# Kernel tuning notes

Hardware: AMD Instinct MI355X
Metric: run time of the kernel (lower is better)

The kernel has to match this reference:

```python
import jax, jax.numpy as jnp
import numpy as np

HEADS = 8; DIM = 512; DHEAD = 64; INNER = HEADS * DHEAD
QB = 4; NTOK = 1024
GAMMA = 0.01; LAMBDA_REG = 0.001


def _ln(x, g, b, eps=1e-5):
    mu = x.mean(axis=-1, keepdims=True)
    var = x.var(axis=-1, keepdims=True)
    return (x - mu) / jnp.sqrt(var + eps) * g + b


def setup_inputs() -> dict:
    key = jax.random.key(0)
    ks = jax.random.split(key, 12)
    def w(k, shape, scale=0.02):
        return jax.random.normal(k, shape, dtype=jnp.float32) * scale
    return {
        'q': jax.random.normal(ks[0], (QB, NTOK, DIM), dtype=jnp.float32),
        'k': jax.random.normal(ks[1], (QB, NTOK, DIM), dtype=jnp.float32),
        'v': jax.random.normal(ks[2], (QB, NTOK, DIM), dtype=jnp.float32),
        'ln_in_g': jnp.ones((DIM,), jnp.float32),
        'ln_in_b': jnp.zeros((DIM,), jnp.float32),
        'W_in': w(ks[3], (DIM, INNER)),
        'wp_W1': w(ks[4], (2 * DHEAD, DHEAD)),
        'wp_b1': jnp.zeros((DHEAD,), jnp.float32),
        'wp_ln_g': jnp.ones((DHEAD,), jnp.float32),
        'wp_ln_b': jnp.zeros((DHEAD,), jnp.float32),
        'wp_W2': w(ks[5], (DHEAD, DHEAD // 2)),
        'wp_b2': jnp.zeros((DHEAD // 2,), jnp.float32),
        'wp_W3': w(ks[6], (DHEAD // 2, 3)),
        'wp_b3': jnp.zeros((3,), jnp.float32),
        'weight_temp': jnp.ones((1,), jnp.float32),
        'W_out': w(ks[7], (INNER, DIM)),
        'b_out': jnp.zeros((DIM,), jnp.float32),
    }


def _forward(q, k, v, ln_in_g, ln_in_b, W_in, wp_W1, wp_b1, wp_ln_g, wp_ln_b,
             wp_W2, wp_b2, wp_W3, wp_b3, weight_temp, W_out, b_out):
    def proj(t):  # [Q,N,DIM] -> [h,Q,N,d]
        y = _ln(t, ln_in_g, ln_in_b) @ W_in
        return y.reshape(t.shape[0], t.shape[1], HEADS, DHEAD).transpose(2, 0, 1, 3)
    f_q, f_k, f_v = proj(q), proj(k), proj(v)
    m = f_k.shape[2]
    sg = jax.lax.stop_gradient

    # --- cosine distance (clamped) ---
    dots = jnp.einsum('hqnd,hqmd->hqnm', f_q, f_k)
    n1 = jnp.linalg.norm(f_q, axis=-1, keepdims=True) + 1e-8   # [h,q,n,1]
    n2 = jnp.linalg.norm(f_k, axis=-1, keepdims=True) + 1e-8   # [h,q,m,1]
    cos = jnp.clip(dots / (n1 * jnp.swapaxes(n2, -1, -2)), -0.99, 0.99)

    # --- regularized covariance ---
    fkc = f_k - f_k.mean(axis=2, keepdims=True)
    fqc = f_q - f_q.mean(axis=-1, keepdims=True)
    cov = jnp.einsum('hqnd,hqmd->hqnm', fqc, fkc) / (DHEAD ** 0.5 + 1e-6)
    base_reg = LAMBDA_REG / max(m, 1)
    reg = jnp.where(jnp.std(cov, ddof=1) < 1e-6, base_reg * 10.0, base_reg)
    cov = jnp.clip(reg * cov, -50.0, 50.0)

    # --- margin-based variance (eval mode: adaptive_gamma = gamma) ---
    qn = f_q / jnp.maximum(jnp.linalg.norm(f_q, axis=-1, keepdims=True), 1e-6)
    kn = f_k / jnp.maximum(jnp.linalg.norm(f_k, axis=-1, keepdims=True), 1e-6)
    csim = jnp.clip(jnp.einsum('hqnd,hqmd->hqnm', qn, kn), -0.99, 0.99)
    margin = jnp.clip(GAMMA - csim, 0.0, 10.0)
    var_c = jnp.broadcast_to(margin.mean(axis=-1, keepdims=True), csim.shape)

    # --- dynamic per-head weight predictor (dropout off in eval) ---
    qg = f_q.mean(axis=(1, 2))          # [h,d]
    kg = f_k.mean(axis=(1, 2))
    feats = jnp.concatenate([qg, kg], axis=-1)          # [h,2d]
    h1 = jax.nn.relu(_ln(feats @ wp_W1 + wp_b1, wp_ln_g, wp_ln_b))
    h2 = jax.nn.relu(h1 @ wp_W2 + wp_b2)
    logits = jax.nn.softmax(h2 @ wp_W3 + wp_b3, axis=-1)  # Sequential ends with Softmax
    wt = jnp.clip(weight_temp, 0.1, 20.0)
    w = jax.nn.softmax(logits / wt, axis=-1)
    w = jnp.clip(w, 0.05, 0.8)
    w = w / w.sum(axis=-1, keepdims=True)                # [h,3]
    cw = w[:, 0].reshape(HEADS, 1, 1, 1)
    covw = w[:, 1].reshape(HEADS, 1, 1, 1)
    vw = w[:, 2].reshape(HEADS, 1, 1, 1)

    # --- normalize each component by its (detached) global std ---
    cn = sg(jnp.std(cos, ddof=1)) + 1e-6
    covn = sg(jnp.std(cov, ddof=1)) + 1e-6
    vn = sg(jnp.std(var_c, ddof=1)) + 1e-6
    cscale = jnp.where(cn < 1e-4, 0.1, 1.0)
    d2 = cw * (cos / cn * cscale) + covw * (cov / covn * 0.5) + vw * (var_c / vn * 0.5)
    dstd = jnp.std(d2, ddof=1)
    temp = jnp.where(dstd < 1e-6, 0.1, 0.3 + sg(dstd))
    d2 = d2 / jnp.clip(temp, 0.1, 5.0)

    attn = jax.nn.softmax(d2, axis=-1)
    out = jnp.einsum('hqnm,hqmd->hqnd', attn, f_v)
    out = out.transpose(1, 2, 0, 3).reshape(out.shape[1], out.shape[2], INNER)
    return out @ W_out + b_out


def reference(q, k, v, ln_in_g, ln_in_b, W_in, wp_W1, wp_b1, wp_ln_g, wp_ln_b,
              wp_W2, wp_b2, wp_W3, wp_b3, weight_temp, W_out, b_out):
    return _forward(q, k, v, ln_in_g, ln_in_b, W_in, wp_W1, wp_b1, wp_ln_g, wp_ln_b,
                    wp_W2, wp_b2, wp_W3, wp_b3, weight_temp, W_out, b_out)
```

## Files before the change

kernel.cpp:

```cpp
#include <hip/hip_runtime.h>
#include <math.h>

#define NH    8
#define NQB   4
#define NPAIR 32
#define NTOK  1024
#define DH    64
#define DIMX  512
#define NROWS (NPAIR*NTOK)

typedef __attribute__((ext_vector_type(8))) short short8;
typedef _Float16 half8 __attribute__((ext_vector_type(8)));
typedef __attribute__((ext_vector_type(4))) float f32x4;

__device__ __forceinline__ unsigned short f2bf(float x){
  unsigned u = __float_as_uint(x);
  u += 0x7fffu + ((u>>16)&1u);
  return (unsigned short)(u>>16);
}
__device__ __forceinline__ float bf2f(unsigned short h){
  return __uint_as_float(((unsigned)h)<<16);
}
__device__ __forceinline__ unsigned short f2h(float x){
  union{ _Float16 f; unsigned short u; } c; c.f = (_Float16)x; return c.u;
// ... 9 lines not shown
}
__device__ __forceinline__ void dma16(const void* g, void* l){
  __builtin_amdgcn_global_load_lds(
      (const __attribute__((address_space(1))) void*)g,
      (__attribute__((address_space(3))) void*)l, 16, 0, 0);
}

__device__ __forceinline__ size_t cidx(int r, int c){
  return ((((size_t)((r>>6)*8 + (c>>6)))*8 + ((c&63)>>3))*64 + (r&63))*8 + (c&7);
}
__device__ __forceinline__ size_t kidx(int p, int key, int dh){
  return ((((size_t)(p*16 + (key>>6)))*8 + (dh>>3))*64 + (key&63))*8 + (dh&7);
}


__global__ __launch_bounds__(256) void k_lnstats(const float* __restrict__ q,
    const float* __restrict__ k, const float* __restrict__ v,
    float* __restrict__ mu_rstd){
  int wid = threadIdx.x >> 6, lane = threadIdx.x & 63;
  int tok = blockIdx.x*4 + wid;
  const float* src = (tok < 4096) ? q : ((tok < 8192) ? k : v);
  int t = tok & 4095;
  const float4* p4 = (const float4*)(src + (size_t)t*DIMX) + lane*2;
  float4 a = p4[0], b = p4[1];
  float s  = a.x+a.y+a.z+a.w + b.x+b.y+b.z+b.w;
  float ss = a.x*a.x+a.y*a.y+a.z*a.z+a.w*a.w
           + b.x*b.x+b.y*b.y+b.z*b.z+b.w*b.w;
  #pragma unroll
  for (int off=32; off; off>>=1){ s += __shfl_down(s,off); ss += __shfl_down(ss,off); }
  if (lane==0){
    float mu = s*(1.0f/512.0f);
    float var = ss*(1.0f/512.0f) - mu*mu;
    mu_rstd[tok*2+0] = mu;
    mu_rstd[tok*2+1] = 1.0f/sqrtf(var + 1e-5f);
  }
}


__global__ __launch_bounds__(256) void k_splitW(const float* __restrict__ Wa,
    const float* __restrict__ Wb,
    unsigned short* __restrict__ Wth, unsigned short* __restrict__ Wtl,
    unsigned short* __restrict__ Woth, unsigned short* __restrict__ Wotl){
  __shared__ float tile[64][65];
  int z = blockIdx.z;
  const float* W = z ? Wb : Wa;
  unsigned short* oh_ = z ? Woth : Wth;
  unsigned short* ol_ = z ? Wotl : Wtl;
  int kb = blockIdx.x, nb = blockIdx.y, tid = threadIdx.x;
  #pragma unroll
  for (int it=0; it<4; ++it){
    int idx = tid + 256*it;
    int kr = idx>>4, c4 = idx&15;
    float4 vv = *(const float4*)(W + (size_t)(kb*64+kr)*DIMX + nb*64 + c4*4);
    tile[c4*4+0][kr]=vv.x; tile[c4*4+1][kr]=vv.y; tile[c4*4+2][kr]=vv.z; tile[c4*4+3][kr]=vv.w;
  }
  __syncthreads();
  #pragma unroll
  for (int it=0; it<4; ++it){
    int idx = tid + 256*it;
    int n = idx>>4, k4 = idx&15;
    size_t base = cidx(nb*64+n, kb*64+k4*4);
    ushort4 hv, lv;
    { float xx=tile[n][k4*4+0]; unsigned short hh=f2bf(xx); hv.x=hh; lv.x=f2bf(xx-bf2f(hh)); }
    { float xx=tile[n][k4*4+1]; unsigned short hh=f2bf(xx); hv.y=hh; lv.y=f2bf(xx-bf2f(hh)); }
    { float xx=tile[n][k4*4+2]; unsigned short hh=f2bf(xx); hv.z=hh; lv.z=f2bf(xx-bf2f(hh)); }
    { float xx=tile[n][k4*4+3]; unsigned short hh=f2bf(xx); hv.w=hh; lv.w=f2bf(xx-bf2f(hh)); }
    *(ushort4*)(oh_+base) = hv;
    *(ushort4*)(ol_+base) = lv;
  }
}


__global__ __launch_bounds__(256) void k_projmm(
    const float* __restrict__ q, const float* __restrict__ k, const float* __restrict__ v,
    const float* __restrict__ g, const float* __restrict__ bln,
    const unsigned short* __restrict__ Wth, const unsigned short* __restrict__ Wtl,
    const float* __restrict__ mu_rstd,
    unsigned short* __restrict__ fqh, unsigned short* __restrict__ fql,
    unsigned short* __restrict__ fkh, unsigned short* __restrict__ fkl,
    float* __restrict__ fv,
    double* __restrict__ qgs, double* __restrict__ nusum){
  __shared__ __align__(16) unsigned short Ahs[64*72];
  __shared__ __align__(16) unsigned short Als[64*72];
// ... 130 lines not shown
      for (int nt=0;nt<4;++nt){
        #pragma unroll
        for (int i=0;i<4;++i){
          int tglob = mb*64 + rbase + mt*16 + qd*4 + i;
          int qb = tglob>>10, n = tglob&1023;
          int p = head*4 + qb;
          int d = nt*16 + lm;
          fv[((size_t)(p*NTOK+n))*DH + d] = acc[mt][nt][i];
        }
      }
    }
  }
}


__global__ __launch_bounds__(256) void k_vT(const float* __restrict__ fv,
    unsigned short* __restrict__ fvTh, unsigned short* __restrict__ fvTl){
  __shared__ float tile[64][65];
  int mc = blockIdx.x, p = blockIdx.y, tid = threadIdx.x;
  #pragma unroll
  for (int it=0; it<4; ++it){
    int idx = tid + 256*it;
    int m = idx>>4, d4 = idx&15;
    float4 vv = *(const float4*)(fv + ((size_t)(p*NTOK + mc*64 + m)*DH + d4*4));
    tile[d4*4+0][m]=vv.x; tile[d4*4+1][m]=vv.y; tile[d4*4+2][m]=vv.z; tile[d4*4+3][m]=vv.w;
  }
  __syncthreads();
  #pragma unroll
  for (int it=0; it<2; ++it){
    int idx = tid + 256*it;
    int d = idx>>3, seg = idx&7;
    size_t base = ((((size_t)(p*16+mc))*8 + seg)*64 + d)*8;
    ushort4 h0,h1,l0,l1;
    { float xx=tile[d][seg*8+0]; unsigned short hh=f2h(xx); h0.x=hh; l0.x=f2h(xx-h2f(hh)); }
    { float xx=tile[d][seg*8+1]; unsigned short hh=f2h(xx); h0.y=hh; l0.y=f2h(xx-h2f(hh)); }
    { float xx=tile[d][seg*8+2]; unsigned short hh=f2h(xx); h0.z=hh; l0.z=f2h(xx-h2f(hh)); }
    { float xx=tile[d][seg*8+3]; unsigned short hh=f2h(xx); h0.w=hh; l0.w=f2h(xx-h2f(hh)); }
    { float xx=tile[d][seg*8+4]; unsigned short hh=f2h(xx); h1.x=hh; l1.x=f2h(xx-h2f(hh)); }
    { float xx=tile[d][seg*8+5]; unsigned short hh=f2h(xx); h1.y=hh; l1.y=f2h(xx-h2f(hh)); }
    { float xx=tile[d][seg*8+6]; unsigned short hh=f2h(xx); h1.z=hh; l1.z=f2h(xx-h2f(hh)); }
    { float xx=tile[d][seg*8+7]; unsigned short hh=f2h(xx); h1.w=hh; l1.w=f2h(xx-h2f(hh)); }
    *(ushort4*)(fvTh+base)   = h0;
    *(ushort4*)(fvTh+base+4) = h1;
    *(ushort4*)(fvTl+base)   = l0;
    *(ushort4*)(fvTl+base+4) = l1;
  }
}


__global__ __launch_bounds__(256) void k_rows(
    const unsigned short* __restrict__ fqh, const unsigned short* __restrict__ fql,
    const unsigned short* __restrict__ fkh, const unsigned short* __restrict__ fkl,
    const double* __restrict__ nusum,
    float* __restrict__ inv_na_q, float* __restrict__ muqA, float* __restrict__ tqA,
    float* __restrict__ inv_na_k, float* __restrict__ skA){
  int wid = threadIdx.x >> 6, lane = threadIdx.x & 63;
  int row = blockIdx.x*4 + wid;
  int p = row >> 10;
  int key = row & 1023;
  size_t ix = (size_t)row*DH + lane;
  float xq = bf2f(fqh[ix]) + bf2f(fql[ix]);
  float nv = (float)(nusum[(size_t)p*DH + lane] * (1.0/1024.0));
  float s = xq, ss = xq*xq, sd = xq*nv;
  #pragma unroll
  for (int off=32; off; off>>=1){
    s += __shfl_down(s,off); ss += __shfl_down(ss,off); sd += __shfl_down(sd,off);
  }
  if (lane==0){
    float nrm = sqrtf(ss);
    inv_na_q[row] = 1.0f/(nrm+1e-8f);
    muqA[row] = s*(1.0f/64.0f);
    tqA[row] = sd;
  }
  size_t ixk = kidx(p, key, lane);
  float xk = bf2f(fkh[ixk]) + bf2f(fkl[ixk]);
  float s2 = xk, ss2 = xk*xk;
  #pragma unroll
  for (int off=32; off; off>>=1){
    s2 += __shfl_down(s2,off); ss2 += __shfl_down(ss2,off);
  }
  if (lane==0){
    float nrm = sqrtf(ss2);
    inv_na_k[row] = 1.0f/(nrm+1e-8f);
    skA[row] = s2;
  }
}


__global__ __launch_bounds__(256) void k_wp(const double* __restrict__ qgs,
    const double* __restrict__ nusum,
    const float* __restrict__ W1, const float* __restrict__ b1,
    const float* __restrict__ lgv, const float* __restrict__ lbv,
    const float* __restrict__ W2, const float* __restrict__ b2,
    const float* __restrict__ W3, const float* __restrict__ b3,
    const float* __restrict__ wtemp, float* __restrict__ wp_out,
    float* __restrict__ Sarr){
  __shared__ float feats[8][128];
  __shared__ float h1[8][64];
  __shared__ float h2s[8][32];
  __shared__ float lgt[8][3];
  __shared__ float mv[8][2];
  int tid = threadIdx.x;
  for (int idx = tid; idx < 1024; idx += 256){
    int h = idx >> 7, i = idx & 127;
    double vv;
    if (i < 64){
      vv = qgs[h*64+i];
    } else {
      int d = i - 64;
      vv = nusum[(size_t)(h*4+0)*DH+d] + nusum[(size_t)(h*4+1)*DH+d]
         + nusum[(size_t)(h*4+2)*DH+d] + nusum[(size_t)(h*4+3)*DH+d];
    }
    feats[h][i] = (float)(vv * (1.0/4096.0));
  }
  if (tid < 32){
    double s = 0.0;
    for (int d = 0; d < 64; ++d) s += nusum[(size_t)tid*DH + d];
    Sarr[tid] = (float)(s * (1.0/1024.0));
  }
  __syncthreads();
  for (int idx = tid; idx < 512; idx += 256){
    int h = idx >> 6, j = idx & 63;
    float s = b1[j];
    for (int i = 0; i < 128; ++i) s += feats[h][i]*W1[i*64+j];
    h1[h][j] = s;
  }
  __syncthreads();
  if (tid < 8){
    float s=0.f, ss=0.f;
    for (int j=0;j<64;++j){ float vv=h1[tid][j]; s+=vv; ss+=vv*vv; }
    float mu = s*(1.0f/64.0f);
    float var = ss*(1.0f/64.0f)-mu*mu;
    mv[tid][0]=mu; mv[tid][1]=1.0f/sqrtf(var+1e-5f);
  }
  __syncthreads();
  for (int idx = tid; idx < 512; idx += 256){
    int h = idx>>6, j = idx&63;
    float vv = (h1[h][j]-mv[h][0])*mv[h][1]*lgv[j] + lbv[j];
    h1[h][j] = fmaxf(vv, 0.f);
  }
  __syncthreads();
  {
    int h = tid >> 5, j = tid & 31;
    float s = b2[j];
    for (int i=0;i<64;++i) s += h1[h][i]*W2[i*32+j];
    h2s[h][j] = fmaxf(s, 0.f);
  }
  __syncthreads();
  if (tid < 24){
    int h = tid/3, j = tid - h*3;
    float s = b3[j];
    for (int i=0;i<32;++i) s += h2s[h][i]*W3[i*3+j];
    lgt[h][j] = s;
  }
  __syncthreads();
  if (tid < 8){
    int h = tid;
    float z0=lgt[h][0], z1=lgt[h][1], z2=lgt[h][2];
    float m = fmaxf(z0,fmaxf(z1,z2));
    float e0=expf(z0-m), e1=expf(z1-m), e2=expf(z2-m);
    float inv = 1.0f/(e0+e1+e2);
    float l0=e0*inv, l1=e1*inv, l2=e2*inv;
    float wt = fminf(fmaxf(wtemp[0], 0.1f), 20.0f);
    float y0=l0/wt, y1=l1/wt, y2=l2/wt;
    float m2 = fmaxf(y0,fmaxf(y1,y2));
    float f0=expf(y0-m2), f1=expf(y1-m2), f2=expf(y2-m2);
    float inv2 = 1.0f/(f0+f1+f2);
    float w0=f0*inv2, w1=f1*inv2, w2=f2*inv2;
    w0 = fminf(fmaxf(w0,0.05f),0.8f);
    w1 = fminf(fmaxf(w1,0.05f),0.8f);
    w2 = fminf(fmaxf(w2,0.05f),0.8f);
    float isum = 1.0f/(w0+w1+w2);
    wp_out[h*3+0]=w0*isum; wp_out[h*3+1]=w1*isum; wp_out[h*3+2]=w2*isum;
  }
}


__global__ __launch_bounds__(256) void k_passA(
    const unsigned short* __restrict__ fqh, const unsigned short* __restrict__ fql,
    const unsigned short* __restrict__ fkh, const unsigned short* __restrict__ fkl,
    const float* __restrict__ inv_na_q, const float* __restrict__ muqA,
    const float* __restrict__ tqA,
    const float* __restrict__ inv_na_k, const float* __restrict__ skA,
    const float* __restrict__ Sarr,
    float* __restrict__ rs_cos, float* __restrict__ rs_cov, float* __restrict__ rs_marg,
    float* __restrict__ mxcosA, float* __restrict__ mxcovA,
    double* __restrict__ gacc){
  __shared__ float redbuf[4][16][5];
  __shared__ double wredS[4][3];
  int b = blockIdx.x;
  int p = ((b&7)<<2) | ((b>>3)&3);
  int s = b>>5;
  int n0 = s*32;
  int tid = threadIdx.x, w = tid>>6, l = tid&63;
  int lm = l&15, q = l>>4;
  int rt = w&1, cw = w>>1;
  int nw = n0 + rt*16;
  float Sp = Sarr[p];
  const float inv8 = (float)(1.0/(8.0+1e-6));
  float ia[4], m8[4], t8[4];
  #pragma unroll
  for (int i=0;i<4;++i){
// ... 95 lines not shown
    double vv = vals[c2];
    #pragma unroll
    for (int off=32; off; off>>=1) vv += __shfl_down(vv, off);
    if (l==0) wredS[w][c2] = vv;
  }
  __syncthreads();
  if (tid < 32){
    int rt2 = tid>>4, r16 = tid&15;
    int w0 = rt2, w1 = rt2+2;
    float sc = redbuf[w0][r16][0]+redbuf[w1][r16][0];
    float sv = redbuf[w0][r16][1]+redbuf[w1][r16][1];
    float sm = redbuf[w0][r16][2]+redbuf[w1][r16][2];
    float mxc = fmaxf(redbuf[w0][r16][3],redbuf[w1][r16][3]);
    float mxv = fmaxf(redbuf[w0][r16][4],redbuf[w1][r16][4]);
    int row = p*NTOK + n0 + tid;
    rs_cos[row]=sc; rs_cov[row]=sv; rs_marg[row]=sm;
    mxcosA[row]=mxc; mxcovA[row]=mxv;
  }
  if (tid == 0){
    int h = p >> 2;
    #pragma unroll
    for (int c2=0;c2<3;++c2){
      double t = wredS[0][c2]+wredS[1][c2]+wredS[2][c2]+wredS[3][c2];
      atomicAdd(&gacc[h*3+c2], t);
    }
  }
}


__global__ __launch_bounds__(256) void k_rowfin(const float* __restrict__ rs_cos,
    const float* __restrict__ rs_cov, const float* __restrict__ rs_marg,
    float* __restrict__ var_row, double* __restrict__ racc){
  __shared__ double wredS[4][6];
  int row = blockIdx.x*256 + threadIdx.x;
  int p = row >> 10; int h = p >> 2;
  float vr = rs_marg[row] * (1.0f/1024.0f);
  var_row[row] = vr;
  double dv = (double)vr;
  double rc = (double)rs_cos[row], rv = (double)rs_cov[row];
  double vals[6];
  vals[0] = 1024.0*dv;
  vals[1] = 1024.0*dv*dv;
  vals[2] = dv*rc;
  vals[3] = dv*rv;
  vals[4] = rc;
  vals[5] = rv;
  int lane = threadIdx.x & 63, wid = threadIdx.x >> 6;
  #pragma unroll
  for (int c2 = 0; c2 < 6; ++c2){
    double vv = vals[c2];
    #pragma unroll
    for (int off=32; off; off>>=1) vv += __shfl_down(vv, off);
    if (lane==0) wredS[wid][c2] = vv;
  }
  __syncthreads();
  if (threadIdx.x == 0){
    #pragma unroll
    for (int c2 = 0; c2 < 6; ++c2){
      double t = wredS[0][c2]+wredS[1][c2]+wredS[2][c2]+wredS[3][c2];
      atomicAdd(&racc[h*6+c2], t);
    }
  }
}


__global__ void k_final(const double* __restrict__ gacc, const double* __restrict__ racc,
                        const float* __restrict__ wp_out, float* __restrict__ coef){
  if (threadIdx.x != 0) return;
  const double N = 33554432.0;
  double Sc1=0,Sc2=0,Sv1=0,Sv2=0,Sr1=0,Sr2=0;
  for (int h=0;h<8;++h){
    Sc2+=gacc[h*3+0]; Sv2+=gacc[h*3+1];
    Sr1+=racc[h*6+0]; Sr2+=racc[h*6+1];
    Sc1+=racc[h*6+4]; Sv1+=racc[h*6+5];
  }
  double cvar = (Sc2 - Sc1*Sc1/N)/(N-1.0);
  double cn = sqrt(fmax(cvar,0.0)) + 1e-6;
  double cscale = (cn < 1e-4) ? 0.1 : 1.0;
  double vraw = (Sv2 - Sv1*Sv1/N)/(N-1.0);
  double sraw = sqrt(fmax(vraw,0.0));
  double basev = 0.001/1024.0;
  double regv = (sraw < 1e-6) ? basev*10.0 : basev;
  double covn = regv*sraw + 1e-6;
  double vvar = (Sr2 - Sr1*Sr1/N)/(N-1.0);
  double vn = sqrt(fmax(vvar,0.0)) + 1e-6;
  double ah[8], bh[8], chh[8];
  double Sd1=0.0, Sd2=0.0;
  for (int h=0;h<8;++h){
    double a = (double)wp_out[h*3+0]/cn*cscale;
    double b = (double)wp_out[h*3+1]*regv*0.5/covn;
    double c = (double)wp_out[h*3+2]*0.5/vn;
    ah[h]=a; bh[h]=b; chh[h]=c;
    Sd1 += a*racc[h*6+4] + b*racc[h*6+5] + c*racc[h*6+0];
    Sd2 += a*a*gacc[h*3+0] + b*b*gacc[h*3+1] + c*c*racc[h*6+1]
         + 2.0*(a*b*gacc[h*3+2] + a*c*racc[h*6+2] + b*c*racc[h*6+3]);
  }
  double dvar = (Sd2 - Sd1*Sd1/N)/(N-1.0);
  double dstd = sqrt(fmax(dvar,0.0));
  double temp = (dstd < 1e-6) ? 0.1 : 0.3 + dstd;
  double tcl = fmin(fmax(temp,0.1),5.0);
  double it = 1.0/tcl;
  for (int h=0;h<8;++h){
    coef[h*3+0] = (float)(ah[h]*it);
    coef[h*3+1] = (float)(bh[h]*it);
    coef[h*3+2] = (float)(chh[h]*it);
  }
}


__global__ __launch_bounds__(256) void k_pv(
    const unsigned short* __restrict__ fqh, const unsigned short* __restrict__ fql,
    const unsigned short* __restrict__ fkh, const unsigned short* __restrict__ fkl,
    const unsigned short* __restrict__ fvTh, const unsigned short* __restrict__ fvTl,
    const float* __restrict__ inv_na_q, const float* __restrict__ muqA,
    const float* __restrict__ tqA,
    const float* __restrict__ inv_na_k, const float* __restrict__ skA,
    const float* __restrict__ Sarr, const float* __restrict__ var_row,
    const float* __restrict__ mxcosA, const float* __restrict__ mxcovA,
    const float* __restrict__ coef,
    unsigned short* __restrict__ ohh, unsigned short* __restrict__ ohl){
  __shared__ __align__(16) unsigned short ph[2][32][72];
  __shared__ float denbuf[4][16];
  __shared__ float dnv[32];
  int b = blockIdx.x;
  int p = ((b&7)<<2) | ((b>>3)&3);
  int s = b>>5;
  int n0 = s*32;
  int h = p>>2, qb = p&3;
  int tid = threadIdx.x, w = tid>>6, l = tid&63;
  int lm = l&15, q = l>>4;
  int rt = w&1, cw = w>>1;
  int nw = n0 + rt*16;
  float A = coef[h*3+0], B = coef[h*3+1], C = coef[h*3+2];
  float Sp = Sarr[p];
  const float inv8 = (float)(1.0/(8.0+1e-6));
  float B8 = B*inv8;
  float ia[4], bm[4], o2[4];
  #pragma unroll
  for (int i=0;i<4;++i){
    int rg = p*NTOK + nw + q*4 + i;
    float mq = muqA[rg];
    ia[i] = inv_na_q[rg];
    bm[i] = B8*mq;
    float tq2 = tqA[rg] - mq*Sp;
    float vr = var_row[rg];
    float Mh = A*mxcosA[rg] + B*mxcovA[rg] + C*vr;
    o2[i] = (C*vr - Mh) - B8*tq2;
  }
// ... 63 lines not shown
    half8 pb10 = *(const half8*)&phc_[16+lm][q*8]; \
    half8 pb11 = *(const half8*)&phc_[16+lm][32+q*8]; \
    o0 = mfma16f(vh0,pb00,o0); o0 = mfma16f(vl0,pb00,o0); \
    o0 = mfma16f(vh1,pb01,o0); o0 = mfma16f(vl1,pb01,o0); \
    o1 = mfma16f(vh0,pb10,o1); o1 = mfma16f(vl0,pb10,o1); \
    o1 = mfma16f(vh1,pb11,o1); o1 = mfma16f(vl1,pb11,o1); \
  }while(0)

  short8 KA[8], KB[8];
  PV_KLOAD(KA, c0);
  for (int t = 0; t < 16; t += 2){
    int ccA = (t + c0) & 15;
    int ccB = (t + 1 + c0) & 15;
    PV_KLOAD(KB, ccB);
    {
      unsigned short (*phc)[72] = ph[0];
      PV_QK(KA, ccA, phc);
      PV_TAIL(ccA, phc);
    }
    if (t < 14){
      int ccA2 = (t + 2 + c0) & 15;
      PV_KLOAD(KA, ccA2);
    }
    {
      unsigned short (*phc)[72] = ph[1];
      PV_QK(KB, ccB, phc);
      PV_TAIL(ccB, phc);
    }
  }
#undef PV_KLOAD
#undef PV_QK
#undef PV_TAIL

  #pragma unroll
  for (int m=1;m<16;m<<=1){
    #pragma unroll
    for (int i=0;i<4;++i) den[i] += __shfl_xor(den[i],m);
  }
  if (lm==0){
    #pragma unroll
// ... 149 lines not shown
  char* wsb = (char*)d_ws;
  double* gacc = (double*)wsb;
  double* racc = gacc + 24;
  double* qgs  = racc + 48;
  double* nusum= qgs + 512;
  float* fvA = (float*)(wsb + 24576);
  unsigned short* ohh = (unsigned short*)fvA;
  unsigned short* ohl = ohh + (size_t)NQB*NTOK*NH*DH;
  float* mu_rstd = fvA + (size_t)NPAIR*NTOK*DH;
  float* Sarr = mu_rstd + 24576;
  float* inv_na_q = Sarr + 64;
  float* muqA     = inv_na_q + NROWS;
  float* tqA      = muqA + NROWS;
  float* inv_na_k = tqA + NROWS;
  float* skA      = inv_na_k + NROWS;
  float* rs_cos   = skA + NROWS;
  float* rs_cov   = rs_cos + NROWS;
  float* rs_marg  = rs_cov + NROWS;
  float* var_row  = rs_marg + NROWS;
  float* mxcos    = var_row + NROWS;
  float* mxcov    = mxcos + NROWS;
  float* wp_out   = mxcov + NROWS;
  float* coef     = wp_out + 32;
  float* endf     = coef + 32;
  size_t off16 = (size_t)((char*)endf - wsb);
  off16 = (off16 + 63) & ~(size_t)63;
  unsigned short* fqh  = (unsigned short*)(wsb + off16);
  unsigned short* fql  = fqh  + (size_t)NPAIR*NTOK*DH;
  unsigned short* fkh  = fql  + (size_t)NPAIR*NTOK*DH;
  unsigned short* fkl  = fkh  + (size_t)NPAIR*NTOK*DH;
  unsigned short* fvTh = fkl  + (size_t)NPAIR*NTOK*DH;
  unsigned short* fvTl = fvTh + (size_t)NPAIR*NTOK*DH;
  unsigned short* Wth  = fvTl + (size_t)NPAIR*NTOK*DH;
  unsigned short* Wtl  = Wth  + (size_t)DIMX*DIMX;
  unsigned short* Woth = Wtl  + (size_t)DIMX*DIMX;
  unsigned short* Wotl = Woth + (size_t)DIMX*DIMX;
  size_t need = (size_t)((char*)(Wotl + (size_t)DIMX*DIMX) - wsb);
  if (ws_size < need) return;

  hipMemsetAsync(wsb, 0, 24576, stream);
  k_lnstats<<<3072, 256, 0, stream>>>(q, k, v, mu_rstd);
  k_splitW<<<dim3(8,8,2), 256, 0, stream>>>(W_in, W_out, Wth, Wtl, Woth, Wotl);
  k_projmm<<<dim3(64,4,3), 256, 0, stream>>>(q, k, v, ln_g, ln_b, Wth, Wtl,
                                             mu_rstd, fqh, fql, fkh, fkl, fvA,
                                             qgs, nusum);
  k_vT<<<dim3(16,32), 256, 0, stream>>>(fvA, fvTh, fvTl);
  k_rows<<<8192, 256, 0, stream>>>(fqh, fql, fkh, fkl, nusum,
                                   inv_na_q, muqA, tqA, inv_na_k, skA);
  k_wp<<<1, 256, 0, stream>>>(qgs, nusum, wp_W1, wp_b1, wp_lg, wp_lb,
                              wp_W2, wp_b2, wp_W3, wp_b3, wtemp, wp_out, Sarr);
  k_passA<<<1024, 256, 0, stream>>>(fqh, fql, fkh, fkl,
                                    inv_na_q, muqA, tqA, inv_na_k, skA, Sarr,
                                    rs_cos, rs_cov, rs_marg,
                                    mxcos, mxcov, gacc);
  k_rowfin<<<128, 256, 0, stream>>>(rs_cos, rs_cov, rs_marg, var_row, racc);
  k_final<<<1, 64, 0, stream>>>(gacc, racc, wp_out, coef);
  k_pv<<<1024, 256, 0, stream>>>(fqh, fql, fkh, fkl, fvTh, fvTl,
                                 inv_na_q, muqA, tqA, inv_na_k, skA, Sarr,
                                 var_row, mxcos, mxcov, coef,
                                 ohh, ohl);
  k_outmm<<<dim3(64,4), 256, 0, stream>>>(ohh, ohl, Woth, Wotl, b_out, out);
}
```

Before: 253.9 us.

## Merge small kernels to cut launch count and fold final stats into consumers

Merges the LN-stats kernel, weight split and the workspace memset into one launch. Also merges the V transpose, row-stats and weight-predictor kernels into a second launch. Moves the row-finalisation reductions into passA and recomputes the final coefficients per block inside k_pv, which drops k_rowfin and k_final and their intermediate arrays. It also pads the P tile's LDS rows from 72 to 76. Fewer launches and less global round-tripping are traded for redundant coefficient math per PV block and more divergent heterogeneous blocks.

```diff
diff --git a/kernel.cpp b/kernel.cpp
--- a/kernel.cpp
+++ b/kernel.cpp
@@ -47,59 +47,65 @@
 }
 
 
-__global__ __launch_bounds__(256) void k_lnstats(const float* __restrict__ q,
-    const float* __restrict__ k, const float* __restrict__ v,
-    float* __restrict__ mu_rstd){
-  int wid = threadIdx.x >> 6, lane = threadIdx.x & 63;
-  int tok = blockIdx.x*4 + wid;
-  const float* src = (tok < 4096) ? q : ((tok < 8192) ? k : v);
-  int t = tok & 4095;
-  const float4* p4 = (const float4*)(src + (size_t)t*DIMX) + lane*2;
-  float4 a = p4[0], b = p4[1];
-  float s  = a.x+a.y+a.z+a.w + b.x+b.y+b.z+b.w;
-  float ss = a.x*a.x+a.y*a.y+a.z*a.z+a.w*a.w
-           + b.x*b.x+b.y*b.y+b.z*b.z+b.w*b.w;
-  #pragma unroll
-  for (int off=32; off; off>>=1){ s += __shfl_down(s,off); ss += __shfl_down(ss,off); }
-  if (lane==0){
-    float mu = s*(1.0f/512.0f);
-    float var = ss*(1.0f/512.0f) - mu*mu;
-    mu_rstd[tok*2+0] = mu;
-    mu_rstd[tok*2+1] = 1.0f/sqrtf(var + 1e-5f);
-  }
-}
-
-
-__global__ __launch_bounds__(256) void k_splitW(const float* __restrict__ Wa,
-    const float* __restrict__ Wb,
+__global__ __launch_bounds__(256) void k_pre(
+    const float* __restrict__ q, const float* __restrict__ k, const float* __restrict__ v,
+    float* __restrict__ mu_rstd,
+    const float* __restrict__ Wa, const float* __restrict__ Wb,
     unsigned short* __restrict__ Wth, unsigned short* __restrict__ Wtl,
-    unsigned short* __restrict__ Woth, unsigned short* __restrict__ Wotl){
+    unsigned short* __restrict__ Woth, unsigned short* __restrict__ Wotl,
+    float* __restrict__ zacc){
   __shared__ float tile[64][65];
-  int z = blockIdx.z;
-  const float* W = z ? Wb : Wa;
-  unsigned short* oh_ = z ? Woth : Wth;
-  unsigned short* ol_ = z ? Wotl : Wtl;
-  int kb = blockIdx.x, nb = blockIdx.y, tid = threadIdx.x;
-  #pragma unroll
-  for (int it=0; it<4; ++it){
-    int idx = tid + 256*it;
-    int kr = idx>>4, c4 = idx&15;
-    float4 vv = *(const float4*)(W + (size_t)(kb*64+kr)*DIMX + nb*64 + c4*4);
-    tile[c4*4+0][kr]=vv.x; tile[c4*4+1][kr]=vv.y; tile[c4*4+2][kr]=vv.z; tile[c4*4+3][kr]=vv.w;
-  }
-  __syncthreads();
-  #pragma unroll
-  for (int it=0; it<4; ++it){
-    int idx = tid + 256*it;
-    int n = idx>>4, k4 = idx&15;
-    size_t base = cidx(nb*64+n, kb*64+k4*4);
-    ushort4 hv, lv;
-    { float xx=tile[n][k4*4+0]; unsigned short hh=f2bf(xx); hv.x=hh; lv.x=f2bf(xx-bf2f(hh)); }
-    { float xx=tile[n][k4*4+1]; unsigned short hh=f2bf(xx); hv.y=hh; lv.y=f2bf(xx-bf2f(hh)); }
-    { float xx=tile[n][k4*4+2]; unsigned short hh=f2bf(xx); hv.z=hh; lv.z=f2bf(xx-bf2f(hh)); }
-    { float xx=tile[n][k4*4+3]; unsigned short hh=f2bf(xx); hv.w=hh; lv.w=f2bf(xx-bf2f(hh)); }
-    *(ushort4*)(oh_+base) = hv;
-    *(ushort4*)(ol_+base) = lv;
+  int b = blockIdx.x, tid = threadIdx.x;
+  if (b < 3072){
+    int wid = tid >> 6, lane = tid & 63;
+    int tok = b*4 + wid;
+    const float* src = (tok < 4096) ? q : ((tok < 8192) ? k : v);
+    int t = tok & 4095;
+    const float4* p4 = (const float4*)(src + (size_t)t*DIMX) + lane*2;
+    float4 a = p4[0], bb = p4[1];
+    float s  = a.x+a.y+a.z+a.w + bb.x+bb.y+bb.z+bb.w;
+    float ss = a.x*a.x+a.y*a.y+a.z*a.z+a.w*a.w
+             + bb.x*bb.x+bb.y*bb.y+bb.z*bb.z+bb.w*bb.w;
+    #pragma unroll
+    for (int off=32; off; off>>=1){ s += __shfl_down(s,off); ss += __shfl_down(ss,off); }
+    if (lane==0){
+      float mu = s*(1.0f/512.0f);
+      float var = ss*(1.0f/512.0f) - mu*mu;
+      mu_rstd[tok*2+0] = mu;
+      mu_rstd[tok*2+1] = 1.0f/sqrtf(var + 1e-5f);
+    }
+  } else if (b < 3200){
+    int sb = b - 3072;
+    int z = sb >> 6, rem = sb & 63, kb = rem & 7, nb = rem >> 3;
+    const float* W = z ? Wb : Wa;
+    unsigned short* oh_ = z ? Woth : Wth;
+    unsigned short* ol_ = z ? Wotl : Wtl;
+    #pragma unroll
+    for (int it=0; it<4; ++it){
+      int idx = tid + 256*it;
+      int kr = idx>>4, c4 = idx&15;
+      float4 vv = *(const float4*)(W + (size_t)(kb*64+kr)*DIMX + nb*64 + c4*4);
+      tile[c4*4+0][kr]=vv.x; tile[c4*4+1][kr]=vv.y; tile[c4*4+2][kr]=vv.z; tile[c4*4+3][kr]=vv.w;
+    }
+    __syncthreads();
+    #pragma unroll
+    for (int it=0; it<4; ++it){
+      int idx = tid + 256*it;
+      int n = idx>>4, k4 = idx&15;
+      size_t base = cidx(nb*64+n, kb*64+k4*4);
+      ushort4 hv, lv;
+      { float xx=tile[n][k4*4+0]; unsigned short hh=f2bf(xx); hv.x=hh; lv.x=f2bf(xx-bf2f(hh)); }
+      { float xx=tile[n][k4*4+1]; unsigned short hh=f2bf(xx); hv.y=hh; lv.y=f2bf(xx-bf2f(hh)); }
+      { float xx=tile[n][k4*4+2]; unsigned short hh=f2bf(xx); hv.z=hh; lv.z=f2bf(xx-bf2f(hh)); }
+      { float xx=tile[n][k4*4+3]; unsigned short hh=f2bf(xx); hv.w=hh; lv.w=f2bf(xx-bf2f(hh)); }
+      *(ushort4*)(oh_+base) = hv;
+      *(ushort4*)(ol_+base) = lv;
+    }
+  } else {
+    uint4 z4 = {0u,0u,0u,0u};
+    uint4* dst = (uint4*)zacc;
+    #pragma unroll
+    for (int i=0;i<6;++i) dst[tid + 256*i] = z4;
   }
 }
 
@@ -260,164 +266,163 @@
 }
 
 
-__global__ __launch_bounds__(256) void k_vT(const float* __restrict__ fv,
-    unsigned short* __restrict__ fvTh, unsigned short* __restrict__ fvTl){
-  __shared__ float tile[64][65];
-  int mc = blockIdx.x, p = blockIdx.y, tid = threadIdx.x;
-  #pragma unroll
-  for (int it=0; it<4; ++it){
-    int idx = tid + 256*it;
-    int m = idx>>4, d4 = idx&15;
-    float4 vv = *(const float4*)(fv + ((size_t)(p*NTOK + mc*64 + m)*DH + d4*4));
-    tile[d4*4+0][m]=vv.x; tile[d4*4+1][m]=vv.y; tile[d4*4+2][m]=vv.z; tile[d4*4+3][m]=vv.w;
-  }
-  __syncthreads();
-  #pragma unroll
-  for (int it=0; it<2; ++it){
-    int idx = tid + 256*it;
-    int d = idx>>3, seg = idx&7;
-    size_t base = ((((size_t)(p*16+mc))*8 + seg)*64 + d)*8;
-    ushort4 h0,h1,l0,l1;
-    { float xx=tile[d][seg*8+0]; unsigned short hh=f2h(xx); h0.x=hh; l0.x=f2h(xx-h2f(hh)); }
-    { float xx=tile[d][seg*8+1]; unsigned short hh=f2h(xx); h0.y=hh; l0.y=f2h(xx-h2f(hh)); }
-    { float xx=tile[d][seg*8+2]; unsigned short hh=f2h(xx); h0.z=hh; l0.z=f2h(xx-h2f(hh)); }
-    { float xx=tile[d][seg*8+3]; unsigned short hh=f2h(xx); h0.w=hh; l0.w=f2h(xx-h2f(hh)); }
-    { float xx=tile[d][seg*8+4]; unsigned short hh=f2h(xx); h1.x=hh; l1.x=f2h(xx-h2f(hh)); }
-    { float xx=tile[d][seg*8+5]; unsigned short hh=f2h(xx); h1.y=hh; l1.y=f2h(xx-h2f(hh)); }
-    { float xx=tile[d][seg*8+6]; unsigned short hh=f2h(xx); h1.z=hh; l1.z=f2h(xx-h2f(hh)); }
-    { float xx=tile[d][seg*8+7]; unsigned short hh=f2h(xx); h1.w=hh; l1.w=f2h(xx-h2f(hh)); }
-    *(ushort4*)(fvTh+base)   = h0;
-    *(ushort4*)(fvTh+base+4) = h1;
-    *(ushort4*)(fvTl+base)   = l0;
-    *(ushort4*)(fvTl+base+4) = l1;
-  }
-}
-
-
-__global__ __launch_bounds__(256) void k_rows(
+__global__ __launch_bounds__(256) void k_mid(
+    const float* __restrict__ fv,
+    unsigned short* __restrict__ fvTh, unsigned short* __restrict__ fvTl,
     const unsigned short* __restrict__ fqh, const unsigned short* __restrict__ fql,
     const unsigned short* __restrict__ fkh, const unsigned short* __restrict__ fkl,
     const double* __restrict__ nusum,
     float* __restrict__ inv_na_q, float* __restrict__ muqA, float* __restrict__ tqA,
-    float* __restrict__ inv_na_k, float* __restrict__ skA){
-  int wid = threadIdx.x >> 6, lane = threadIdx.x & 63;
-  int row = blockIdx.x*4 + wid;
-  int p = row >> 10;
-  int key = row & 1023;
-  size_t ix = (size_t)row*DH + lane;
-  float xq = bf2f(fqh[ix]) + bf2f(fql[ix]);
-  float nv = (float)(nusum[(size_t)p*DH + lane] * (1.0/1024.0));
-  float s = xq, ss = xq*xq, sd = xq*nv;
-  #pragma unroll
-  for (int off=32; off; off>>=1){
-    s += __shfl_down(s,off); ss += __shfl_down(ss,off); sd += __shfl_down(sd,off);
-  }
-  if (lane==0){
-    float nrm = sqrtf(ss);
-    inv_na_q[row] = 1.0f/(nrm+1e-8f);
-    muqA[row] = s*(1.0f/64.0f);
-    tqA[row] = sd;
-  }
-  size_t ixk = kidx(p, key, lane);
-  float xk = bf2f(fkh[ixk]) + bf2f(fkl[ixk]);
-  float s2 = xk, ss2 = xk*xk;
-  #pragma unroll
-  for (int off=32; off; off>>=1){
-    s2 += __shfl_down(s2,off); ss2 += __shfl_down(ss2,off);
-  }
-  if (lane==0){
-    float nrm = sqrtf(ss2);
-    inv_na_k[row] = 1.0f/(nrm+1e-8f);
-    skA[row] = s2;
-  }
-}
-
-
-__global__ __launch_bounds__(256) void k_wp(const double* __restrict__ qgs,
-    const double* __restrict__ nusum,
+    float* __restrict__ inv_na_k, float* __restrict__ skA,
+    const double* __restrict__ qgs,
     const float* __restrict__ W1, const float* __restrict__ b1,
     const float* __restrict__ lgv, const float* __restrict__ lbv,
     const float* __restrict__ W2, const float* __restrict__ b2,
     const float* __restrict__ W3, const float* __restrict__ b3,
     const float* __restrict__ wtemp, float* __restrict__ wp_out,
     float* __restrict__ Sarr){
-  __shared__ float feats[8][128];
-  __shared__ float h1[8][64];
-  __shared__ float h2s[8][32];
-  __shared__ float lgt[8][3];
-  __shared__ float mv[8][2];
-  int tid = threadIdx.x;
-  for (int idx = tid; idx < 1024; idx += 256){
-    int h = idx >> 7, i = idx & 127;
-    double vv;
-    if (i < 64){
-      vv = qgs[h*64+i];
-    } else {
-      int d = i - 64;
-      vv = nusum[(size_t)(h*4+0)*DH+d] + nusum[(size_t)(h*4+1)*DH+d]
-         + nusum[(size_t)(h*4+2)*DH+d] + nusum[(size_t)(h*4+3)*DH+d];
-    }
-    feats[h][i] = (float)(vv * (1.0/4096.0));
-  }
-  if (tid < 32){
-    double s = 0.0;
-    for (int d = 0; d < 64; ++d) s += nusum[(size_t)tid*DH + d];
-    Sarr[tid] = (float)(s * (1.0/1024.0));
-  }
-  __syncthreads();
-  for (int idx = tid; idx < 512; idx += 256){
-    int h = idx >> 6, j = idx & 63;
-    float s = b1[j];
-    for (int i = 0; i < 128; ++i) s += feats[h][i]*W1[i*64+j];
-    h1[h][j] = s;
-  }
-  __syncthreads();
-  if (tid < 8){
-    float s=0.f, ss=0.f;
-    for (int j=0;j<64;++j){ float vv=h1[tid][j]; s+=vv; ss+=vv*vv; }
-    float mu = s*(1.0f/64.0f);
-    float var = ss*(1.0f/64.0f)-mu*mu;
-    mv[tid][0]=mu; mv[tid][1]=1.0f/sqrtf(var+1e-5f);
-  }
-  __syncthreads();
-  for (int idx = tid; idx < 512; idx += 256){
-    int h = idx>>6, j = idx&63;
-    float vv = (h1[h][j]-mv[h][0])*mv[h][1]*lgv[j] + lbv[j];
-    h1[h][j] = fmaxf(vv, 0.f);
-  }
-  __syncthreads();
-  {
-    int h = tid >> 5, j = tid & 31;
-    float s = b2[j];
-    for (int i=0;i<64;++i) s += h1[h][i]*W2[i*32+j];
-    h2s[h][j] = fmaxf(s, 0.f);
-  }
-  __syncthreads();
-  if (tid < 24){
-    int h = tid/3, j = tid - h*3;
-    float s = b3[j];
-    for (int i=0;i<32;++i) s += h2s[h][i]*W3[i*3+j];
-    lgt[h][j] = s;
-  }
-  __syncthreads();
-  if (tid < 8){
-    int h = tid;
-    float z0=lgt[h][0], z1=lgt[h][1], z2=lgt[h][2];
-    float m = fmaxf(z0,fmaxf(z1,z2));
-    float e0=expf(z0-m), e1=expf(z1-m), e2=expf(z2-m);
-    float inv = 1.0f/(e0+e1+e2);
-    float l0=e0*inv, l1=e1*inv, l2=e2*inv;
-    float wt = fminf(fmaxf(wtemp[0], 0.1f), 20.0f);
-    float y0=l0/wt, y1=l1/wt, y2=l2/wt;
-    float m2 = fmaxf(y0,fmaxf(y1,y2));
-    float f0=expf(y0-m2), f1=expf(y1-m2), f2=expf(y2-m2);
-    float inv2 = 1.0f/(f0+f1+f2);
-    float w0=f0*inv2, w1=f1*inv2, w2=f2*inv2;
-    w0 = fminf(fmaxf(w0,0.05f),0.8f);
-    w1 = fminf(fmaxf(w1,0.05f),0.8f);
-    w2 = fminf(fmaxf(w2,0.05f),0.8f);
-    float isum = 1.0f/(w0+w1+w2);
-    wp_out[h*3+0]=w0*isum; wp_out[h*3+1]=w1*isum; wp_out[h*3+2]=w2*isum;
+  __shared__ __align__(16) float msm[64*65];
+  int b = blockIdx.x, tid = threadIdx.x;
+  if (b < 512){
+    float (*tile)[65] = (float(*)[65])msm;
+    int mc = b & 15, p = b >> 4;
+    #pragma unroll
+    for (int it=0; it<4; ++it){
+      int idx = tid + 256*it;
+      int m = idx>>4, d4 = idx&15;
+      float4 vv = *(const float4*)(fv + ((size_t)(p*NTOK + mc*64 + m)*DH + d4*4));
+      tile[d4*4+0][m]=vv.x; tile[d4*4+1][m]=vv.y; tile[d4*4+2][m]=vv.z; tile[d4*4+3][m]=vv.w;
+    }
+    __syncthreads();
+    #pragma unroll
+    for (int it=0; it<2; ++it){
+      int idx = tid + 256*it;
+      int d = idx>>3, seg = idx&7;
+      size_t base = ((((size_t)(p*16+mc))*8 + seg)*64 + d)*8;
+      ushort4 h0,h1v,l0,l1;
+      { float xx=tile[d][seg*8+0]; unsigned short hh=f2h(xx); h0.x=hh; l0.x=f2h(xx-h2f(hh)); }
+      { float xx=tile[d][seg*8+1]; unsigned short hh=f2h(xx); h0.y=hh; l0.y=f2h(xx-h2f(hh)); }
+      { float xx=tile[d][seg*8+2]; unsigned short hh=f2h(xx); h0.z=hh; l0.z=f2h(xx-h2f(hh)); }
+      { float xx=tile[d][seg*8+3]; unsigned short hh=f2h(xx); h0.w=hh; l0.w=f2h(xx-h2f(hh)); }
+      { float xx=tile[d][seg*8+4]; unsigned short hh=f2h(xx); h1v.x=hh; l1.x=f2h(xx-h2f(hh)); }
+      { float xx=tile[d][seg*8+5]; unsigned short hh=f2h(xx); h1v.y=hh; l1.y=f2h(xx-h2f(hh)); }
+      { float xx=tile[d][seg*8+6]; unsigned short hh=f2h(xx); h1v.z=hh; l1.z=f2h(xx-h2f(hh)); }
+      { float xx=tile[d][seg*8+7]; unsigned short hh=f2h(xx); h1v.w=hh; l1.w=f2h(xx-h2f(hh)); }
+      *(ushort4*)(fvTh+base)   = h0;
+      *(ushort4*)(fvTh+base+4) = h1v;
+      *(ushort4*)(fvTl+base)   = l0;
+      *(ushort4*)(fvTl+base+4) = l1;
+    }
+  } else if (b < 8704){
+    int rb = b - 512;
+    int wid = tid >> 6, lane = tid & 63;
+    int row = rb*4 + wid;
+    int p = row >> 10;
+    int key = row & 1023;
+    size_t ix = (size_t)row*DH + lane;
+    float xq = bf2f(fqh[ix]) + bf2f(fql[ix]);
+    float nv = (float)(nusum[(size_t)p*DH + lane] * (1.0/1024.0));
+    float s = xq, ss = xq*xq, sd = xq*nv;
+    #pragma unroll
+    for (int off=32; off; off>>=1){
+      s += __shfl_down(s,off); ss += __shfl_down(ss,off); sd += __shfl_down(sd,off);
+    }
+    if (lane==0){
+      float nrm = sqrtf(ss);
+      inv_na_q[row] = 1.0f/(nrm+1e-8f);
+      muqA[row] = s*(1.0f/64.0f);
+      tqA[row] = sd;
+    }
+    size_t ixk = kidx(p, key, lane);
+    float xk = bf2f(fkh[ixk]) + bf2f(fkl[ixk]);
+    float s2 = xk, ss2 = xk*xk;
+    #pragma unroll
+    for (int off=32; off; off>>=1){
+      s2 += __shfl_down(s2,off); ss2 += __shfl_down(ss2,off);
+    }
+    if (lane==0){
+      float nrm = sqrtf(ss2);
+      inv_na_k[row] = 1.0f/(nrm+1e-8f);
+      skA[row] = s2;
+    }
+  } else {
+    float* feats = msm;
+    float* h1    = msm + 1024;
+    float* h2s   = msm + 1536;
+    float* lgt   = msm + 1792;
+    float* mv    = msm + 1832;
+    for (int idx = tid; idx < 1024; idx += 256){
+      int h = idx >> 7, i = idx & 127;
+      double vv;
+      if (i < 64){
+        vv = qgs[h*64+i];
+      } else {
+        int d = i - 64;
+        vv = nusum[(size_t)(h*4+0)*DH+d] + nusum[(size_t)(h*4+1)*DH+d]
+           + nusum[(size_t)(h*4+2)*DH+d] + nusum[(size_t)(h*4+3)*DH+d];
+      }
+      feats[h*128+i] = (float)(vv * (1.0/4096.0));
+    }
+    if (tid < 32){
+      double s = 0.0;
+      for (int d = 0; d < 64; ++d) s += nusum[(size_t)tid*DH + d];
+      Sarr[tid] = (float)(s * (1.0/1024.0));
+    }
+    __syncthreads();
+    for (int idx = tid; idx < 512; idx += 256){
+      int h = idx >> 6, j = idx & 63;
+      float s = b1[j];
+      for (int i = 0; i < 128; ++i) s += feats[h*128+i]*W1[i*64+j];
+      h1[h*64+j] = s;
+    }
+    __syncthreads();
+    if (tid < 8){
+      float s=0.f, ss=0.f;
+      for (int j=0;j<64;++j){ float vv=h1[tid*64+j]; s+=vv; ss+=vv*vv; }
+      float mu = s*(1.0f/64.0f);
+      float var = ss*(1.0f/64.0f)-mu*mu;
+      mv[tid*2+0]=mu; mv[tid*2+1]=1.0f/sqrtf(var+1e-5f);
+    }
+    __syncthreads();
+    for (int idx = tid; idx < 512; idx += 256){
+      int h = idx>>6, j = idx&63;
+      float vv = (h1[h*64+j]-mv[h*2+0])*mv[h*2+1]*lgv[j] + lbv[j];
+      h1[h*64+j] = fmaxf(vv, 0.f);
+    }
+    __syncthreads();
+    {
+      int h = tid >> 5, j = tid & 31;
+      float s = b2[j];
+      for (int i=0;i<64;++i) s += h1[h*64+i]*W2[i*32+j];
+      h2s[h*32+j] = fmaxf(s, 0.f);
+    }
+    __syncthreads();
+    if (tid < 24){
+      int h = tid/3, j = tid - h*3;
+      float s = b3[j];
+      for (int i=0;i<32;++i) s += h2s[h*32+i]*W3[i*3+j];
+      lgt[h*3+j] = s;
+    }
+    __syncthreads();
+    if (tid < 8){
+      int h = tid;
+      float z0=lgt[h*3+0], z1=lgt[h*3+1], z2=lgt[h*3+2];
+      float m = fmaxf(z0,fmaxf(z1,z2));
+      float e0=expf(z0-m), e1=expf(z1-m), e2=expf(z2-m);
+      float inv = 1.0f/(e0+e1+e2);
+      float l0=e0*inv, l1=e1*inv, l2=e2*inv;
+      float wt = fminf(fmaxf(wtemp[0], 0.1f), 20.0f);
+      float y0=l0/wt, y1=l1/wt, y2=l2/wt;
+      float m2 = fmaxf(y0,fmaxf(y1,y2));
+      float f0=expf(y0-m2), f1=expf(y1-m2), f2=expf(y2-m2);
+      float inv2 = 1.0f/(f0+f1+f2);
+      float w0=f0*inv2, w1=f1*inv2, w2=f2*inv2;
+      w0 = fminf(fmaxf(w0,0.05f),0.8f);
+      w1 = fminf(fmaxf(w1,0.05f),0.8f);
+      w2 = fminf(fmaxf(w2,0.05f),0.8f);
+      float isum = 1.0f/(w0+w1+w2);
+      wp_out[h*3+0]=w0*isum; wp_out[h*3+1]=w1*isum; wp_out[h*3+2]=w2*isum;
+    }
   }
 }
 
@@ -429,9 +434,9 @@
     const float* __restrict__ tqA,
     const float* __restrict__ inv_na_k, const float* __restrict__ skA,
     const float* __restrict__ Sarr,
-    float* __restrict__ rs_cos, float* __restrict__ rs_cov, float* __restrict__ rs_marg,
+    float* __restrict__ var_row,
     float* __restrict__ mxcosA, float* __restrict__ mxcovA,
-    double* __restrict__ gacc){
+    double* __restrict__ gacc, double* __restrict__ racc){
   __shared__ float redbuf[4][16][5];
   __shared__ double wredS[4][3];
   int b = blockIdx.x;
@@ -557,8 +562,29 @@
     float mxc = fmaxf(redbuf[w0][r16][3],redbuf[w1][r16][3]);
     float mxv = fmaxf(redbuf[w0][r16][4],redbuf[w1][r16][4]);
     int row = p*NTOK + n0 + tid;
-    rs_cos[row]=sc; rs_cov[row]=sv; rs_marg[row]=sm;
-    mxcosA[row]=mxc; mxcovA[row]=mxv;
+    float vr = sm * (1.0f/1024.0f);
+    var_row[row] = vr;
+    mxcosA[row] = mxc; mxcovA[row] = mxv;
+    double dv = (double)vr;
+    double rc = (double)sc, rv = (double)sv;
+    double vals2[6];
+    vals2[0] = 1024.0*dv;
+    vals2[1] = 1024.0*dv*dv;
+    vals2[2] = dv*rc;
+    vals2[3] = dv*rv;
+    vals2[4] = rc;
+    vals2[5] = rv;
+    int hh = p >> 2;
+    #pragma unroll
+    for (int c2 = 0; c2 < 6; ++c2){
+      double vv = vals2[c2];
+      vv += __shfl_down(vv,16);
+      vv += __shfl_down(vv,8);
+      vv += __shfl_down(vv,4);
+      vv += __shfl_down(vv,2);
+      vv += __shfl_down(vv,1);
+      if (tid==0) atomicAdd(&racc[hh*6+c2], vv);
+    }
   }
   if (tid == 0){
     int h = p >> 2;
@@ -567,86 +593,6 @@
       double t = wredS[0][c2]+wredS[1][c2]+wredS[2][c2]+wredS[3][c2];
       atomicAdd(&gacc[h*3+c2], t);
     }
-  }
-}
-
-
-__global__ __launch_bounds__(256) void k_rowfin(const float* __restrict__ rs_cos,
-    const float* __restrict__ rs_cov, const float* __restrict__ rs_marg,
-    float* __restrict__ var_row, double* __restrict__ racc){
-  __shared__ double wredS[4][6];
-  int row = blockIdx.x*256 + threadIdx.x;
-  int p = row >> 10; int h = p >> 2;
-  float vr = rs_marg[row] * (1.0f/1024.0f);
-  var_row[row] = vr;
-  double dv = (double)vr;
-  double rc = (double)rs_cos[row], rv = (double)rs_cov[row];
-  double vals[6];
-  vals[0] = 1024.0*dv;
-  vals[1] = 1024.0*dv*dv;
-  vals[2] = dv*rc;
-  vals[3] = dv*rv;
-  vals[4] = rc;
-  vals[5] = rv;
-  int lane = threadIdx.x & 63, wid = threadIdx.x >> 6;
-  #pragma unroll
-  for (int c2 = 0; c2 < 6; ++c2){
-    double vv = vals[c2];
-    #pragma unroll
-    for (int off=32; off; off>>=1) vv += __shfl_down(vv, off);
-    if (lane==0) wredS[wid][c2] = vv;
-  }
-  __syncthreads();
-  if (threadIdx.x == 0){
-    #pragma unroll
-    for (int c2 = 0; c2 < 6; ++c2){
-      double t = wredS[0][c2]+wredS[1][c2]+wredS[2][c2]+wredS[3][c2];
-      atomicAdd(&racc[h*6+c2], t);
-    }
-  }
-}
-
-
-__global__ void k_final(const double* __restrict__ gacc, const double* __restrict__ racc,
-                        const float* __restrict__ wp_out, float* __restrict__ coef){
-  if (threadIdx.x != 0) return;
-  const double N = 33554432.0;
-  double Sc1=0,Sc2=0,Sv1=0,Sv2=0,Sr1=0,Sr2=0;
-  for (int h=0;h<8;++h){
-    Sc2+=gacc[h*3+0]; Sv2+=gacc[h*3+1];
-    Sr1+=racc[h*6+0]; Sr2+=racc[h*6+1];
-    Sc1+=racc[h*6+4]; Sv1+=racc[h*6+5];
-  }
-  double cvar = (Sc2 - Sc1*Sc1/N)/(N-1.0);
-  double cn = sqrt(fmax(cvar,0.0)) + 1e-6;
-  double cscale = (cn < 1e-4) ? 0.1 : 1.0;
-  double vraw = (Sv2 - Sv1*Sv1/N)/(N-1.0);
-  double sraw = sqrt(fmax(vraw,0.0));
-  double basev = 0.001/1024.0;
-  double regv = (sraw < 1e-6) ? basev*10.0 : basev;
-  double covn = regv*sraw + 1e-6;
-  double vvar = (Sr2 - Sr1*Sr1/N)/(N-1.0);
-  double vn = sqrt(fmax(vvar,0.0)) + 1e-6;
-  double ah[8], bh[8], chh[8];
-  double Sd1=0.0, Sd2=0.0;
-  for (int h=0;h<8;++h){
-    double a = (double)wp_out[h*3+0]/cn*cscale;
-    double b = (double)wp_out[h*3+1]*regv*0.5/covn;
-    double c = (double)wp_out[h*3+2]*0.5/vn;
-    ah[h]=a; bh[h]=b; chh[h]=c;
-    Sd1 += a*racc[h*6+4] + b*racc[h*6+5] + c*racc[h*6+0];
-    Sd2 += a*a*gacc[h*3+0] + b*b*gacc[h*3+1] + c*c*racc[h*6+1]
-         + 2.0*(a*b*gacc[h*3+2] + a*c*racc[h*6+2] + b*c*racc[h*6+3]);
-  }
-  double dvar = (Sd2 - Sd1*Sd1/N)/(N-1.0);
-  double dstd = sqrt(fmax(dvar,0.0));
-  double temp = (dstd < 1e-6) ? 0.1 : 0.3 + dstd;
-  double tcl = fmin(fmax(temp,0.1),5.0);
-  double it = 1.0/tcl;
-  for (int h=0;h<8;++h){
-    coef[h*3+0] = (float)(ah[h]*it);
-    coef[h*3+1] = (float)(bh[h]*it);
-    coef[h*3+2] = (float)(chh[h]*it);
   }
 }
 
@@ -660,11 +606,13 @@
     const float* __restrict__ inv_na_k, const float* __restrict__ skA,
     const float* __restrict__ Sarr, const float* __restrict__ var_row,
     const float* __restrict__ mxcosA, const float* __restrict__ mxcovA,
-    const float* __restrict__ coef,
+    const double* __restrict__ gacc, const double* __restrict__ racc,
+    const float* __restrict__ wp_out,
     unsigned short* __restrict__ ohh, unsigned short* __restrict__ ohl){
-  __shared__ __align__(16) unsigned short ph[2][32][72];
+  __shared__ __align__(16) unsigned short ph[2][32][76];
   __shared__ float denbuf[4][16];
   __shared__ float dnv[32];
+  __shared__ float coefS[3];
   int b = blockIdx.x;
   int p = ((b&7)<<2) | ((b>>3)&3);
   int s = b>>5;
@@ -674,7 +622,46 @@
   int lm = l&15, q = l>>4;
   int rt = w&1, cw = w>>1;
   int nw = n0 + rt*16;
-  float A = coef[h*3+0], B = coef[h*3+1], C = coef[h*3+2];
+  if (tid == 0){
+    const double N = 33554432.0;
+    double Sc1=0,Sc2=0,Sv1=0,Sv2=0,Sr1=0,Sr2=0;
+    for (int hh=0;hh<8;++hh){
+      Sc2+=gacc[hh*3+0]; Sv2+=gacc[hh*3+1];
+      Sr1+=racc[hh*6+0]; Sr2+=racc[hh*6+1];
+      Sc1+=racc[hh*6+4]; Sv1+=racc[hh*6+5];
+    }
+    double cvar = (Sc2 - Sc1*Sc1/N)/(N-1.0);
+    double cn = sqrt(fmax(cvar,0.0)) + 1e-6;
+    double cscale = (cn < 1e-4) ? 0.1 : 1.0;
+    double vraw = (Sv2 - Sv1*Sv1/N)/(N-1.0);
+    double sraw = sqrt(fmax(vraw,0.0));
+    double basev = 0.001/1024.0;
+    double regv = (sraw < 1e-6) ? basev*10.0 : basev;
+    double covn = regv*sraw + 1e-6;
+    double vvar = (Sr2 - Sr1*Sr1/N)/(N-1.0);
+    double vn = sqrt(fmax(vvar,0.0)) + 1e-6;
+    double Sd1=0.0, Sd2=0.0;
+    double ah_=0.0, bh_=0.0, ch_=0.0;
+    for (int hh=0;hh<8;++hh){
+      double a = (double)wp_out[hh*3+0]/cn*cscale;
+      double bcoef = (double)wp_out[hh*3+1]*regv*0.5/covn;
+      double c = (double)wp_out[hh*3+2]*0.5/vn;
+      if (hh==h){ ah_=a; bh_=bcoef; ch_=c; }
+      Sd1 += a*racc[hh*6+4] + bcoef*racc[hh*6+5] + c*racc[hh*6+0];
+      Sd2 += a*a*gacc[hh*3+0] + bcoef*bcoef*gacc[hh*3+1] + c*c*racc[hh*6+1]
+           + 2.0*(a*bcoef*gacc[hh*3+2] + a*c*racc[hh*6+2] + bcoef*c*racc[hh*6+3]);
+    }
+    double dvar = (Sd2 - Sd1*Sd1/N)/(N-1.0);
+    double dstd = sqrt(fmax(dvar,0.0));
+    double temp = (dstd < 1e-6) ? 0.1 : 0.3 + dstd;
+    double tcl = fmin(fmax(temp,0.1),5.0);
+    double it = 1.0/tcl;
+    coefS[0] = (float)(ah_*it);
+    coefS[1] = (float)(bh_*it);
+    coefS[2] = (float)(ch_*it);
+  }
+  __syncthreads();
+  float A = coefS[0], B = coefS[1], C = coefS[2];
   float Sp = Sarr[p];
   const float inv8 = (float)(1.0/(8.0+1e-6));
   float B8 = B*inv8;
@@ -768,7 +755,7 @@
     int ccB = (t + 1 + c0) & 15;
     PV_KLOAD(KB, ccB);
     {
-      unsigned short (*phc)[72] = ph[0];
+      unsigned short (*phc)[76] = ph[0];
       PV_QK(KA, ccA, phc);
       PV_TAIL(ccA, phc);
     }
@@ -777,7 +764,7 @@
       PV_KLOAD(KA, ccA2);
     }
     {
-      unsigned short (*phc)[72] = ph[1];
+      unsigned short (*phc)[76] = ph[1];
       PV_QK(KB, ccB, phc);
       PV_TAIL(ccB, phc);
     }
@@ -957,15 +944,11 @@
   float* tqA      = muqA + NROWS;
   float* inv_na_k = tqA + NROWS;
   float* skA      = inv_na_k + NROWS;
-  float* rs_cos   = skA + NROWS;
-  float* rs_cov   = rs_cos + NROWS;
-  float* rs_marg  = rs_cov + NROWS;
-  float* var_row  = rs_marg + NROWS;
+  float* var_row  = skA + NROWS;
   float* mxcos    = var_row + NROWS;
   float* mxcov    = mxcos + NROWS;
   float* wp_out   = mxcov + NROWS;
-  float* coef     = wp_out + 32;
-  float* endf     = coef + 32;
+  float* endf     = wp_out + 32;
   size_t off16 = (size_t)((char*)endf - wsb);
   off16 = (off16 + 63) & ~(size_t)63;
   unsigned short* fqh  = (unsigned short*)(wsb + off16);
@@ -981,26 +964,22 @@
   size_t need = (size_t)((char*)(Wotl + (size_t)DIMX*DIMX) - wsb);
   if (ws_size < need) return;
 
-  hipMemsetAsync(wsb, 0, 24576, stream);
-  k_lnstats<<<3072, 256, 0, stream>>>(q, k, v, mu_rstd);
-  k_splitW<<<dim3(8,8,2), 256, 0, stream>>>(W_in, W_out, Wth, Wtl, Woth, Wotl);
+  k_pre<<<3201, 256, 0, stream>>>(q, k, v, mu_rstd, W_in, W_out,
+                                  Wth, Wtl, Woth, Wotl, (float*)wsb);
   k_projmm<<<dim3(64,4,3), 256, 0, stream>>>(q, k, v, ln_g, ln_b, Wth, Wtl,
                                              mu_rstd, fqh, fql, fkh, fkl, fvA,
                                              qgs, nusum);
-  k_vT<<<dim3(16,32), 256, 0, stream>>>(fvA, fvTh, fvTl);
-  k_rows<<<8192, 256, 0, stream>>>(fqh, fql, fkh, fkl, nusum,
-                                   inv_na_q, muqA, tqA, inv_na_k, skA);
-  k_wp<<<1, 256, 0, stream>>>(qgs, nusum, wp_W1, wp_b1, wp_lg, wp_lb,
-                              wp_W2, wp_b2, wp_W3, wp_b3, wtemp, wp_out, Sarr);
+  k_mid<<<8705, 256, 0, stream>>>(fvA, fvTh, fvTl, fqh, fql, fkh, fkl, nusum,
+                                  inv_na_q, muqA, tqA, inv_na_k, skA,
+                                  qgs, wp_W1, wp_b1, wp_lg, wp_lb,
+                                  wp_W2, wp_b2, wp_W3, wp_b3, wtemp,
+                                  wp_out, Sarr);
   k_passA<<<1024, 256, 0, stream>>>(fqh, fql, fkh, fkl,
                                     inv_na_q, muqA, tqA, inv_na_k, skA, Sarr,
-                                    rs_cos, rs_cov, rs_marg,
-                                    mxcos, mxcov, gacc);
-  k_rowfin<<<128, 256, 0, stream>>>(rs_cos, rs_cov, rs_marg, var_row, racc);
-  k_final<<<1, 64, 0, stream>>>(gacc, racc, wp_out, coef);
+                                    var_row, mxcos, mxcov, gacc, racc);
   k_pv<<<1024, 256, 0, stream>>>(fqh, fql, fkh, fkl, fvTh, fvTl,
                                  inv_na_q, muqA, tqA, inv_na_k, skA, Sarr,
-                                 var_row, mxcos, mxcov, coef,
+                                 var_row, mxcos, mxcov, gacc, racc, wp_out,
                                  ohh, ohl);
   k_outmm<<<dim3(64,4), 256, 0, stream>>>(ohh, ohl, Woth, Wotl, b_out, out);
 }
```

New measurement: 253.6 us. About the same (-0.1%).
